# Kernel optimization log

Measured on AMD Instinct MI355X. Metric: run time of the kernel, lower is better.

The kernel has to match this reference:

```python
import jax, jax.numpy as jnp
import numpy as np

N, E, H, C, G = 10000, 20000, 12, 768, 64  # nodes, edges, heads, per-head dim, graphs
NEG_SLOPE = 0.2


def _gat_layer(x, W, a_src, a_dst, b, src, dst):
    # x: [N, 768], W: [768, H*C], a_src/a_dst: [H, C], b: [C]
    h = (x @ W).reshape(-1, H, C)                      # [N, H, C]
    s = jnp.einsum('nhc,hc->nh', h, a_src)             # alpha_src per node
    d = jnp.einsum('nhc,hc->nh', h, a_dst)             # alpha_dst per node
    e = jax.nn.leaky_relu(s[src] + d[dst], NEG_SLOPE)  # [Etot, H]
    # segment softmax over incoming edges of each destination node
    m = jax.lax.stop_gradient(jax.ops.segment_max(e, dst, num_segments=N))
    ex = jnp.exp(e - m[dst])
    den = jax.ops.segment_sum(ex, dst, num_segments=N)
    alpha = ex / (den[dst] + 1e-16)                    # [Etot, H]
    out = jax.ops.segment_sum(h[src] * alpha[:, :, None], dst, num_segments=N)
    return out.mean(axis=1) + b                        # concat=False -> head mean, [N, C]


def setup_inputs() -> dict:
    key = jax.random.key(0)
    ks = jax.random.split(key, 16)
    sc = 0.02
    f32 = jnp.float32
    return {
        'x': jax.random.normal(ks[0], (N, 768), f32),
        'edge_index': jax.random.randint(ks[1], (2, E), 0, N),
        'batch': jnp.sort(jax.random.randint(ks[2], (N,), 0, G)),
        'W1': (jax.random.normal(ks[3], (768, H * C), f32) * sc),
        'a_src1': (jax.random.normal(ks[4], (H, C), f32) * sc),
        'a_dst1': (jax.random.normal(ks[5], (H, C), f32) * sc),
        'b1': jnp.zeros((C,), f32),
        'W2': (jax.random.normal(ks[6], (768, H * C), f32) * sc),
        'a_src2': (jax.random.normal(ks[7], (H, C), f32) * sc),
        'a_dst2': (jax.random.normal(ks[8], (H, C), f32) * sc),
        'b2': jnp.zeros((C,), f32),
        'mlp_w1': (jax.random.normal(ks[9], (768, 128), f32) * sc),
        'mlp_b1': jnp.zeros((128,), f32),
        'mlp_w2': (jax.random.normal(ks[10], (128, 4), f32) * sc),
        'mlp_b2': jnp.zeros((4,), f32),
    }


def reference(x, edge_index, batch, W1, a_src1, a_dst1, b1, W2, a_src2, a_dst2, b2,
              mlp_w1, mlp_b1, mlp_w2, mlp_b2):
    loops = jnp.arange(N)                               # GATConv add_self_loops=True
    src = jnp.concatenate([edge_index[0], loops])
    dst = jnp.concatenate([edge_index[1], loops])
    h = _gat_layer(x, W1, a_src1, a_dst1, b1, src, dst)
    h = _gat_layer(h, W2, a_src2, a_dst2, b2, src, dst)
    # scatter_mean over graph assignment
    ssum = jax.ops.segment_sum(h, batch, num_segments=G)
    cnt = jax.ops.segment_sum(jnp.ones((N,), h.dtype), batch, num_segments=G)
    g = ssum / jnp.maximum(cnt, 1.0)[:, None]           # [G, 768]
    z = jax.nn.relu(g @ mlp_w1 + mlp_b1)
    return z @ mlp_w2 + mlp_b2                          # [G, 4] logits
```

## Files before the change

### kernel.cpp

```cpp
#include <hip/hip_runtime.h>
#include <stdint.h>

typedef unsigned short u16;
typedef unsigned int   u32;

#define NNODES 10000
#define NEDGES 20000
#define ETOT   30000
#define NHEADS 12
#define CDIM   768
#define FDIM   768
#define KDIM   9216
#define NGRAPH 64
#define MPAD   10240
#define SPLITS 4
#define KCH    (KDIM / SPLITS)
#define NEG_SLOPE 0.2f
#define DMAX   32

typedef __attribute__((ext_vector_type(8))) short short8;
typedef __attribute__((ext_vector_type(4))) float f32x4;

__device__ __forceinline__ u16 f32_bf16(float f) {
  u32 u = __float_as_uint(f);
  u = (u + 0x7FFFu + ((u >> 16) & 1u)) >> 16;
  return (u16)u;
}

__global__ void k_count(const int* __restrict__ dste, int* __restrict__ counts) {
  int e = blockIdx.x * blockDim.x + threadIdx.x;
  if (e >= ETOT) return;
  int dst;
  if (e < NEDGES) dst = dste[e]; else dst = e - NEDGES;
  atomicAdd(&counts[dst], 1);
}

__global__ void k_scan(const int* __restrict__ counts, int* __restrict__ offs) {
  __shared__ int part[256];
  int t = threadIdx.x;
  const int chunk = 40;
  int beg = t * chunk;
  int end = beg + chunk; if (end > NNODES) end = NNODES;
  int s = 0;
  for (int i = beg; i < end && i < NNODES; i++) s += counts[i];
  part[t] = s;
  __syncthreads();
  for (int d = 1; d < 256; d <<= 1) {
    int v = (t >= d) ? part[t - d] : 0;
    __syncthreads();
    part[t] += v;
    __syncthreads();
  }
  int base = (t == 0) ? 0 : part[t - 1];
  for (int i = beg; i < end && i < NNODES; i++) { offs[i] = base; base += counts[i]; }
  if (t == 255) offs[NNODES] = base;
}

__global__ void k_seed(const int* __restrict__ offs, int* __restrict__ cursor) {
  int n = blockIdx.x * blockDim.x + threadIdx.x;
  if (n < NNODES) cursor[n] = offs[n];
}

__global__ void k_scatter(const int* __restrict__ dste, int* __restrict__ cursor,
                          int* __restrict__ elist) {
  int e = blockIdx.x * blockDim.x + threadIdx.x;
  if (e >= ETOT) return;
  int dst;
  if (e < NEDGES) dst = dste[e]; else dst = e - NEDGES;
  int pos = atomicAdd(&cursor[dst], 1);
  elist[pos] = e;
}

__global__ void k_U(const float* __restrict__ W, const float* __restrict__ a_src,
                    const float* __restrict__ a_dst, float* __restrict__ Ut) {
  int k = blockIdx.x;
  int t = threadIdx.x, w = t >> 6, l = t & 63;
  const float* Wrow = W + (size_t)k * KDIM;
#pragma unroll
  for (int q = 0; q < 6; q++) {
    int o = w * 6 + q;
    int h = (o < 12) ? o : o - 12;
    const float* av = (o < 12) ? (a_src + h * CDIM) : (a_dst + h * CDIM);
    const float* wr = Wrow + h * CDIM;
    float p = 0.f;
    for (int c = l; c < CDIM; c += 64) p += wr[c] * av[c];
#pragma unroll
    for (int d = 32; d > 0; d >>= 1) p += __shfl_down(p, d, 64);
    if (l == 0) Ut[o * FDIM + k] = p;
  }
}

__global__ void k_sd(const float* __restrict__ xin, const float* __restrict__ Ut,
                     float* __restrict__ sd) {
  __shared__ float UtS[24 * FDIM];
  int t = threadIdx.x, w = t >> 6, l = t & 63;
  const float4* U4 = (const float4*)Ut;
  float4* S4 = (float4*)UtS;
  for (int i = t; i < 24 * FDIM / 4; i += 256) S4[i] = U4[i];
  __syncthreads();
#pragma unroll
  for (int rep = 0; rep < 5; rep++) {
    int n = blockIdx.x * 20 + w * 5 + rep;
    if (n >= NNODES) continue;
    const float* xr = xin + (size_t)n * FDIM;
    float4 x0 = *(const float4*)(xr + 4 * l);
    float4 x1 = *(const float4*)(xr + 4 * l + 256);
    float4 x2 = *(const float4*)(xr + 4 * l + 512);
#pragma unroll
    for (int o = 0; o < 24; o++) {
      const float4* up = (const float4*)(UtS + o * FDIM + 4 * l);
      float4 u0 = up[0];
      float4 u1 = up[64];
      float4 u2 = up[128];
      float a = x0.x * u0.x + x0.y * u0.y + x0.z * u0.z + x0.w * u0.w
              + x1.x * u1.x + x1.y * u1.y + x1.z * u1.z + x1.w * u1.w
              + x2.x * u2.x + x2.y * u2.y + x2.z * u2.z + x2.w * u2.w;
#pragma unroll
      for (int d = 32; d > 0; d >>= 1) a += __shfl_xor(a, d, 64);
      if (l == 0) sd[n * 24 + o] = a;
    }
  }
}

__global__ void k_trans(const float* __restrict__ W, u16* __restrict__ Bt) {
  int h = blockIdx.z;
  int kt = blockIdx.x * 32, ct = blockIdx.y * 32;
  int tx = threadIdx.x, ty = threadIdx.y;
  __shared__ float tile[32][33];
#pragma unroll
  for (int r = 0; r < 4; r++)
    tile[ty + 8 * r][tx] = W[(size_t)(kt + ty + 8 * r) * KDIM + h * CDIM + ct + tx];
  __syncthreads();
#pragma unroll
  for (int r = 0; r < 4; r++)
    Bt[(size_t)(ct + ty + 8 * r) * KDIM + h * CDIM + kt + tx] = f32_bf16(tile[tx][ty + 8 * r]);
}

__global__ void k_att(const float* __restrict__ xin, const int* __restrict__ ei,
                      const int* __restrict__ offs, const int* __restrict__ elist,
                      const float* __restrict__ sd, u16* __restrict__ agg) {
  int t = threadIdx.x, w = t >> 6, l = t & 63;
  int n = blockIdx.x * 4 + w;
  __shared__ int   srcsS[4][DMAX];
  __shared__ float alphS[4][NHEADS * DMAX];
  if (n >= NNODES) return;
  int* srcs = srcsS[w];
  float* alph = alphS[w];
  int beg = offs[n];
  int deg = offs[n + 1] - beg;
  if (deg > DMAX) deg = DMAX;
  if (l < deg) {
    int e = elist[beg + l];
    srcs[l] = (e < NEDGES) ? ei[e] : e - NEDGES;
  }
  __builtin_amdgcn_wave_barrier();
  for (int p = l; p < deg * NHEADS; p += 64) {
    int i = p / NHEADS, h = p - i * NHEADS;
    float v = sd[srcs[i] * 24 + h] + sd[n * 24 + 12 + h];
    v = (v > 0.f) ? v : NEG_SLOPE * v;
    alph[h * DMAX + i] = v;
  }
  __builtin_amdgcn_wave_barrier();
  if (l < NHEADS) {
    float m = -1e30f;
    for (int i = 0; i < deg; i++) m = fmaxf(m, alph[l * DMAX + i]);
    float s = 0.f;
    for (int i = 0; i < deg; i++) {
      float ex = expf(alph[l * DMAX + i] - m);
      alph[l * DMAX + i] = ex;
      s += ex;
    }
    float inv = 1.f / (s + 1e-16f);
    for (int i = 0; i < deg; i++) alph[l * DMAX + i] *= inv;
  }
  __builtin_amdgcn_wave_barrier();
  u16* outr = agg + (size_t)n * KDIM + 4 * l;
#pragma unroll
  for (int pass = 0; pass < 3; pass++) {
    float4 acc[NHEADS];
#pragma unroll
    for (int h = 0; h < NHEADS; h++) acc[h] = make_float4(0.f, 0.f, 0.f, 0.f);
    for (int i = 0; i < deg; i++) {
      float4 xv = *(const float4*)(xin + (size_t)srcs[i] * FDIM + pass * 256 + 4 * l);
#pragma unroll
      for (int h = 0; h < NHEADS; h++) {
        float a = alph[h * DMAX + i];
        acc[h].x += a * xv.x; acc[h].y += a * xv.y;
        acc[h].z += a * xv.z; acc[h].w += a * xv.w;
      }
    }
#pragma unroll
    for (int h = 0; h < NHEADS; h++) {
      ushort4 pk;
      pk.x = f32_bf16(acc[h].x); pk.y = f32_bf16(acc[h].y);
      pk.z = f32_bf16(acc[h].z); pk.w = f32_bf16(acc[h].w);
      *(ushort4*)(outr + h * CDIM + pass * 256) = pk;
    }
  }
}

__global__ __launch_bounds__(256, 3) void k_gemm(const u16* __restrict__ A,
    const u16* __restrict__ B, float* __restrict__ C,
    const float* __restrict__ bias, float scale) {
  __shared__ __align__(16) u16 As[2][128 * 32];
  __shared__ __align__(16) u16 Bs[2][128 * 32];
  int t = threadIdx.x;
  int w = t >> 6, l = t & 63;
  int lin = blockIdx.x;
  int xcd = lin & 7;
  int s = lin >> 3;
  int kz = xcd >> 1;
  int colt = (xcd & 1) * 3 + (s % 3);
  int y = s / 3;
  int col0 = colt * 128;
  int row0 = y * 128;
  int kbeg = kz * KCH;
  int wm = (w >> 1) * 64, wn = (w & 1) * 64;
  f32x4 acc[4][4] = {};
  int idx0 = t * 8;
  int idx1 = idx0 + 2048;
  const u16* Ag0 = A + (size_t)(row0 + (idx0 >> 5)) * KDIM + (idx0 & 31) + kbeg;
  const u16* Ag1 = A + (size_t)(row0 + (idx1 >> 5)) * KDIM + (idx1 & 31) + kbeg;
  const u16* Bg0 = B + (size_t)(col0 + (idx0 >> 5)) * KDIM + (idx0 & 31) + kbeg;
  const u16* Bg1 = B + (size_t)(col0 + (idx1 >> 5)) * KDIM + (idx1 & 31) + kbeg;
  int lr = l & 15, lk = (l >> 4) * 8;

  short8 ra0, ra1, rb0, rb1;
  auto gload = [&](int k0) {
    ra0 = *(const short8*)(Ag0 + k0);
    ra1 = *(const short8*)(Ag1 + k0);
    rb0 = *(const short8*)(Bg0 + k0);
    rb1 = *(const short8*)(Bg1 + k0);
  };
  auto swrite = [&](int buf) {
    *(short8*)(&As[buf][idx0]) = ra0;
    *(short8*)(&As[buf][idx1]) = ra1;
    *(short8*)(&Bs[buf][idx0]) = rb0;
    *(short8*)(&Bs[buf][idx1]) = rb1;
  };

  gload(0);
  swrite(0);
  gload(32);
  __syncthreads();
  const int NIT = KCH / 32;
  int cur = 0;
  for (int it = 0; it < NIT; it++) {
    short8 af[4], bf[4];
#pragma unroll
    for (int i = 0; i < 4; i++) af[i] = *(const short8*)(&As[cur][(wm + i * 16 + lr) * 32 + lk]);
#pragma unroll
    for (int j = 0; j < 4; j++) bf[j] = *(const short8*)(&Bs[cur][(wn + j * 16 + lr) * 32 + lk]);
#pragma unroll
    for (int i = 0; i < 4; i++)
#pragma unroll
      for (int j = 0; j < 4; j++)
        acc[i][j] = __builtin_amdgcn_mfma_f32_16x16x32_bf16(af[i], bf[j], acc[i][j], 0, 0, 0);
    if (it + 1 < NIT) {
      swrite(cur ^ 1);
      if (it + 2 < NIT) gload((it + 2) * 32);
    }
    __syncthreads();
    cur ^= 1;
  }

  int lg = l >> 4;
#pragma unroll
  for (int i = 0; i < 4; i++)
#pragma unroll
    for (int j = 0; j < 4; j++) {
      int col = col0 + wn + j * 16 + lr;
      float badd = (kz == 0) ? bias[col] : 0.f;
#pragma unroll
      for (int r = 0; r < 4; r++) {
        int row = row0 + wm + i * 16 + lg * 4 + r;
        unsafeAtomicAdd(&C[(size_t)row * FDIM + col], acc[i][j][r] * scale + badd);
      }
    }
}

__global__ void k_pool(const float* __restrict__ h2, const int* __restrict__ batch,
                       float* __restrict__ g) {
  int gi = blockIdx.x;
  int c = blockIdx.y * 256 + threadIdx.x;
  int lo = 0, hi = NNODES;
  while (lo < hi) { int mid = (lo + hi) >> 1; if (batch[mid] < gi) lo = mid + 1; else hi = mid; }
  int start = lo;
  lo = start; hi = NNODES;
  while (lo < hi) { int mid = (lo + hi) >> 1; if (batch[mid] < gi + 1) lo = mid + 1; else hi = mid; }
  int end = lo;
  int cnt = end - start; if (cnt < 1) cnt = 1;
  float inv = 1.f / (float)cnt;
  float s = 0.f;
  for (int n = start; n < end; n++) s += h2[(size_t)n * FDIM + c];
  g[gi * FDIM + c] = s * inv;
}

__global__ void k_mlp(const float* __restrict__ g, const float* __restrict__ w1,
                      const float* __restrict__ b1, const float* __restrict__ w2,
                      const float* __restrict__ b2, float* __restrict__ out) {
  int gi = blockIdx.x;
  int t = threadIdx.x;
  __shared__ float gs[FDIM];
  __shared__ float zs[128];
  for (int i = t; i < FDIM; i += 128) gs[i] = g[gi * FDIM + i];
  __syncthreads();
  float a = b1[t];
  for (int k = 0; k < FDIM; k++) a += gs[k] * w1[k * 128 + t];
  zs[t] = (a > 0.f) ? a : 0.f;
  __syncthreads();
  if (t < 4) {
    float o = b2[t];
    for (int i = 0; i < 128; i++) o += zs[i] * w2[i * 4 + t];
    out[gi * 4 + t] = o;
  }
}

extern "C" void kernel_launch(void* const* d_in, const int* in_sizes, int n_in,
                              void* d_out, int out_size, void* d_ws, size_t ws_size,
                              hipStream_t stream) {
  const float* x    = (const float*)d_in[0];
  const int*   ei   = (const int*)d_in[1];
  const int*   batch= (const int*)d_in[2];
  const float* W1   = (const float*)d_in[3];
  const float* as1  = (const float*)d_in[4];
  const float* ad1  = (const float*)d_in[5];
  const float* b1   = (const float*)d_in[6];
  const float* W2   = (const float*)d_in[7];
  const float* as2  = (const float*)d_in[8];
  const float* ad2  = (const float*)d_in[9];
  const float* b2   = (const float*)d_in[10];
  const float* mw1  = (const float*)d_in[11];
  const float* mb1  = (const float*)d_in[12];
  const float* mw2  = (const float*)d_in[13];
  const float* mb2  = (const float*)d_in[14];
  float* out = (float*)d_out;
  (void)in_sizes; (void)n_in; (void)out_size; (void)ws_size;

  char* wsb = (char*)d_ws;
  size_t off = 0;
  auto alloc = [&](size_t bytes) -> void* {
    void* p = wsb + off;
    off += (bytes + 255) & ~(size_t)255;
    return p;
  };
  u16*  agg    = (u16*)alloc((size_t)MPAD * KDIM * 2);
  u16*  Bt     = (u16*)alloc((size_t)FDIM * KDIM * 2);
  float* h1    = (float*)alloc((size_t)MPAD * FDIM * 4);
  float* h2    = (float*)alloc((size_t)MPAD * FDIM * 4);
  float* sd    = (float*)alloc((size_t)NNODES * 24 * 4);
  float* Ut    = (float*)alloc((size_t)FDIM * 24 * 4);
  int*  counts = (int*)alloc((size_t)NNODES * 4);
  int*  offs   = (int*)alloc((size_t)(NNODES + 1) * 4);
  int*  cursor = (int*)alloc((size_t)NNODES * 4);
  int*  elist  = (int*)alloc((size_t)ETOT * 4);
  float* gbuf  = (float*)alloc((size_t)NGRAPH * FDIM * 4);

  hipMemsetAsync(counts, 0, NNODES * 4, stream);
  k_count<<<(ETOT + 255) / 256, 256, 0, stream>>>(ei + NEDGES, counts);
  k_scan<<<1, 256, 0, stream>>>(counts, offs);
  k_seed<<<(NNODES + 255) / 256, 256, 0, stream>>>(offs, cursor);
  k_scatter<<<(ETOT + 255) / 256, 256, 0, stream>>>(ei + NEDGES, cursor, elist);

  for (int layer = 0; layer < 2; layer++) {
    const float* xin  = layer ? h1  : x;
    const float* W    = layer ? W2  : W1;
    const float* asrc = layer ? as2 : as1;
    const float* adst = layer ? ad2 : ad1;
    const float* bb   = layer ? b2  : b1;
    float* hout       = layer ? h2  : h1;

    k_U<<<FDIM, 256, 0, stream>>>(W, asrc, adst, Ut);
    k_sd<<<(NNODES + 19) / 20, 256, 0, stream>>>(xin, Ut, sd);
    k_trans<<<dim3(24, 24, 12), dim3(32, 8), 0, stream>>>(W, Bt);
    hipMemsetAsync(hout, 0, (size_t)MPAD * FDIM * 4, stream);
    k_att<<<(NNODES + 3) / 4, 256, 0, stream>>>(xin, ei, offs, elist, sd, agg);
    k_gemm<<<1920, 256, 0, stream>>>(agg, Bt, hout, bb, 1.f / 12.f);
  }

  k_pool<<<dim3(NGRAPH, 3), 256, 0, stream>>>(h2, batch, gbuf);
  k_mlp<<<NGRAPH, 128, 0, stream>>>(gbuf, mw1, mb1, mw2, mb2, out);
}
```

Baseline: 949.2 us.

## Reorder GAT layer to project features before attention aggregation

Projects node features first (x in bf16 times W, giving a bf16 [N, 9216] per-head feature matrix). Attention then gathers these projected per-head rows, does the head-mean and adds the bias directly. This removes the split-K GEMM with float atomics and the output memset. The cost is that the gather now reads full 9216-wide bf16 rows per edge instead of 768-wide fp32 rows, which raises gather traffic. It also rounds the input to bf16 before the projection.

```diff
diff --git a/kernel.cpp b/kernel.cpp
--- a/kernel.cpp
+++ b/kernel.cpp
@@ -12,9 +12,7 @@
 #define FDIM   768
 #define KDIM   9216
 #define NGRAPH 64
-#define MPAD   10240
-#define SPLITS 4
-#define KCH    (KDIM / SPLITS)
+#define MPAD   10112
 #define NEG_SLOPE 0.2f
 #define DMAX   32
 
@@ -25,6 +23,9 @@
   u32 u = __float_as_uint(f);
   u = (u + 0x7FFFu + ((u >> 16) & 1u)) >> 16;
   return (u16)u;
+}
+__device__ __forceinline__ float bf16_f32(u16 v) {
+  return __uint_as_float(((u32)v) << 16);
 }
 
 __global__ void k_count(const int* __restrict__ dste, int* __restrict__ counts) {
@@ -91,7 +92,7 @@
 }
 
 __global__ void k_sd(const float* __restrict__ xin, const float* __restrict__ Ut,
-                     float* __restrict__ sd) {
+                     float* __restrict__ sd, u16* __restrict__ xbf) {
   __shared__ float UtS[24 * FDIM];
   int t = threadIdx.x, w = t >> 6, l = t & 63;
   const float4* U4 = (const float4*)Ut;
@@ -106,6 +107,14 @@
     float4 x0 = *(const float4*)(xr + 4 * l);
     float4 x1 = *(const float4*)(xr + 4 * l + 256);
     float4 x2 = *(const float4*)(xr + 4 * l + 512);
+    u16* xb = xbf + (size_t)n * FDIM + 4 * l;
+    ushort4 p0, p1, p2;
+    p0.x = f32_bf16(x0.x); p0.y = f32_bf16(x0.y); p0.z = f32_bf16(x0.z); p0.w = f32_bf16(x0.w);
+    p1.x = f32_bf16(x1.x); p1.y = f32_bf16(x1.y); p1.z = f32_bf16(x1.z); p1.w = f32_bf16(x1.w);
+    p2.x = f32_bf16(x2.x); p2.y = f32_bf16(x2.y); p2.z = f32_bf16(x2.z); p2.w = f32_bf16(x2.w);
+    *(ushort4*)xb = p0;
+    *(ushort4*)(xb + 256) = p1;
+    *(ushort4*)(xb + 512) = p2;
 #pragma unroll
     for (int o = 0; o < 24; o++) {
       const float4* up = (const float4*)(UtS + o * FDIM + 4 * l);
@@ -123,22 +132,93 @@
 }
 
 __global__ void k_trans(const float* __restrict__ W, u16* __restrict__ Bt) {
-  int h = blockIdx.z;
-  int kt = blockIdx.x * 32, ct = blockIdx.y * 32;
+  int kt = blockIdx.x * 32, jt = blockIdx.y * 32;
   int tx = threadIdx.x, ty = threadIdx.y;
   __shared__ float tile[32][33];
 #pragma unroll
   for (int r = 0; r < 4; r++)
-    tile[ty + 8 * r][tx] = W[(size_t)(kt + ty + 8 * r) * KDIM + h * CDIM + ct + tx];
+    tile[ty + 8 * r][tx] = W[(size_t)(kt + ty + 8 * r) * KDIM + jt + tx];
   __syncthreads();
 #pragma unroll
   for (int r = 0; r < 4; r++)
-    Bt[(size_t)(ct + ty + 8 * r) * KDIM + h * CDIM + kt + tx] = f32_bf16(tile[tx][ty + 8 * r]);
-}
-
-__global__ void k_att(const float* __restrict__ xin, const int* __restrict__ ei,
+    Bt[(size_t)(jt + ty + 8 * r) * FDIM + kt + tx] = f32_bf16(tile[tx][ty + 8 * r]);
+}
+
+__global__ __launch_bounds__(256, 3) void k_gemm(const u16* __restrict__ A,
+    const u16* __restrict__ B, u16* __restrict__ C) {
+  __shared__ __align__(16) u16 As[2][128 * 32];
+  __shared__ __align__(16) u16 Bs[2][128 * 32];
+  int t = threadIdx.x;
+  int w = t >> 6, l = t & 63;
+  int col0 = blockIdx.x * 128;
+  int row0 = blockIdx.y * 128;
+  int wm = (w >> 1) * 64, wn = (w & 1) * 64;
+  f32x4 acc[4][4] = {};
+  int idx0 = t * 8;
+  int idx1 = idx0 + 2048;
+  const u16* Ag0 = A + (size_t)(row0 + (idx0 >> 5)) * FDIM + (idx0 & 31);
+  const u16* Ag1 = A + (size_t)(row0 + (idx1 >> 5)) * FDIM + (idx1 & 31);
+  const u16* Bg0 = B + (size_t)(col0 + (idx0 >> 5)) * FDIM + (idx0 & 31);
+  const u16* Bg1 = B + (size_t)(col0 + (idx1 >> 5)) * FDIM + (idx1 & 31);
+  int lr = l & 15, lk = (l >> 4) * 8;
+
+  short8 ra0, ra1, rb0, rb1;
+  auto gload = [&](int k0) {
+    ra0 = *(const short8*)(Ag0 + k0);
+    ra1 = *(const short8*)(Ag1 + k0);
+    rb0 = *(const short8*)(Bg0 + k0);
+    rb1 = *(const short8*)(Bg1 + k0);
+  };
+  auto swrite = [&](int buf) {
+    *(short8*)(&As[buf][idx0]) = ra0;
+    *(short8*)(&As[buf][idx1]) = ra1;
+    *(short8*)(&Bs[buf][idx0]) = rb0;
+    *(short8*)(&Bs[buf][idx1]) = rb1;
+  };
+
+  gload(0);
+  swrite(0);
+  gload(32);
+  __syncthreads();
+  const int NIT = FDIM / 32;
+  int cur = 0;
+  for (int it = 0; it < NIT; it++) {
+    short8 af[4], bf[4];
+#pragma unroll
+    for (int i = 0; i < 4; i++) af[i] = *(const short8*)(&As[cur][(wm + i * 16 + lr) * 32 + lk]);
+#pragma unroll
+    for (int j = 0; j < 4; j++) bf[j] = *(const short8*)(&Bs[cur][(wn + j * 16 + lr) * 32 + lk]);
+#pragma unroll
+    for (int i = 0; i < 4; i++)
+#pragma unroll
+      for (int j = 0; j < 4; j++)
+        acc[i][j] = __builtin_amdgcn_mfma_f32_16x16x32_bf16(af[i], bf[j], acc[i][j], 0, 0, 0);
+    if (it + 1 < NIT) {
+      swrite(cur ^ 1);
+      if (it + 2 < NIT) gload((it + 2) * 32);
+    }
+    __syncthreads();
+    cur ^= 1;
+  }
+
+  int lg = l >> 4;
+#pragma unroll
+  for (int i = 0; i < 4; i++)
+#pragma unroll
+    for (int j = 0; j < 4; j++) {
+      int col = col0 + wn + j * 16 + lr;
+#pragma unroll
+      for (int r = 0; r < 4; r++) {
+        int row = row0 + wm + i * 16 + lg * 4 + r;
+        C[(size_t)row * KDIM + col] = f32_bf16(acc[i][j][r]);
+      }
+    }
+}
+
+__global__ void k_att(const u16* __restrict__ Hbig, const int* __restrict__ ei,
                       const int* __restrict__ offs, const int* __restrict__ elist,
-                      const float* __restrict__ sd, u16* __restrict__ agg) {
+                      const float* __restrict__ sd, const float* __restrict__ bias,
+                      float* __restrict__ out) {
   int t = threadIdx.x, w = t >> 6, l = t & 63;
   int n = blockIdx.x * 4 + w;
   __shared__ int   srcsS[4][DMAX];
@@ -174,109 +254,30 @@
     for (int i = 0; i < deg; i++) alph[l * DMAX + i] *= inv;
   }
   __builtin_amdgcn_wave_barrier();
-  u16* outr = agg + (size_t)n * KDIM + 4 * l;
 #pragma unroll
   for (int pass = 0; pass < 3; pass++) {
-    float4 acc[NHEADS];
-#pragma unroll
-    for (int h = 0; h < NHEADS; h++) acc[h] = make_float4(0.f, 0.f, 0.f, 0.f);
+    float4 acc = make_float4(0.f, 0.f, 0.f, 0.f);
     for (int i = 0; i < deg; i++) {
-      float4 xv = *(const float4*)(xin + (size_t)srcs[i] * FDIM + pass * 256 + 4 * l);
+      const u16* hb = Hbig + (size_t)srcs[i] * KDIM + pass * 256 + 4 * l;
 #pragma unroll
       for (int h = 0; h < NHEADS; h++) {
+        ushort4 hv = *(const ushort4*)(hb + h * CDIM);
         float a = alph[h * DMAX + i];
-        acc[h].x += a * xv.x; acc[h].y += a * xv.y;
-        acc[h].z += a * xv.z; acc[h].w += a * xv.w;
+        acc.x += a * bf16_f32(hv.x);
+        acc.y += a * bf16_f32(hv.y);
+        acc.z += a * bf16_f32(hv.z);
+        acc.w += a * bf16_f32(hv.w);
       }
     }
-#pragma unroll
-    for (int h = 0; h < NHEADS; h++) {
-      ushort4 pk;
-      pk.x = f32_bf16(acc[h].x); pk.y = f32_bf16(acc[h].y);
-      pk.z = f32_bf16(acc[h].z); pk.w = f32_bf16(acc[h].w);
-      *(ushort4*)(outr + h * CDIM + pass * 256) = pk;
-    }
-  }
-}
-
-__global__ __launch_bounds__(256, 3) void k_gemm(const u16* __restrict__ A,
-    const u16* __restrict__ B, float* __restrict__ C,
-    const float* __restrict__ bias, float scale) {
-  __shared__ __align__(16) u16 As[2][128 * 32];
-  __shared__ __align__(16) u16 Bs[2][128 * 32];
-  int t = threadIdx.x;
-  int w = t >> 6, l = t & 63;
-  int lin = blockIdx.x;
-  int xcd = lin & 7;
-  int s = lin >> 3;
-  int kz = xcd >> 1;
-  int colt = (xcd & 1) * 3 + (s % 3);
-  int y = s / 3;
-  int col0 = colt * 128;
-  int row0 = y * 128;
-  int kbeg = kz * KCH;
-  int wm = (w >> 1) * 64, wn = (w & 1) * 64;
-  f32x4 acc[4][4] = {};
-  int idx0 = t * 8;
-  int idx1 = idx0 + 2048;
-  const u16* Ag0 = A + (size_t)(row0 + (idx0 >> 5)) * KDIM + (idx0 & 31) + kbeg;
-  const u16* Ag1 = A + (size_t)(row0 + (idx1 >> 5)) * KDIM + (idx1 & 31) + kbeg;
-  const u16* Bg0 = B + (size_t)(col0 + (idx0 >> 5)) * KDIM + (idx0 & 31) + kbeg;
-  const u16* Bg1 = B + (size_t)(col0 + (idx1 >> 5)) * KDIM + (idx1 & 31) + kbeg;
-  int lr = l & 15, lk = (l >> 4) * 8;
-
-  short8 ra0, ra1, rb0, rb1;
-  auto gload = [&](int k0) {
-    ra0 = *(const short8*)(Ag0 + k0);
-    ra1 = *(const short8*)(Ag1 + k0);
-    rb0 = *(const short8*)(Bg0 + k0);
-    rb1 = *(const short8*)(Bg1 + k0);
-  };
-  auto swrite = [&](int buf) {
-    *(short8*)(&As[buf][idx0]) = ra0;
-    *(short8*)(&As[buf][idx1]) = ra1;
-    *(short8*)(&Bs[buf][idx0]) = rb0;
-    *(short8*)(&Bs[buf][idx1]) = rb1;
-  };
-
-  gload(0);
-  swrite(0);
-  gload(32);
-  __syncthreads();
-  const int NIT = KCH / 32;
-  int cur = 0;
-  for (int it = 0; it < NIT; it++) {
-    short8 af[4], bf[4];
-#pragma unroll
-    for (int i = 0; i < 4; i++) af[i] = *(const short8*)(&As[cur][(wm + i * 16 + lr) * 32 + lk]);
-#pragma unroll
-    for (int j = 0; j < 4; j++) bf[j] = *(const short8*)(&Bs[cur][(wn + j * 16 + lr) * 32 + lk]);
-#pragma unroll
-    for (int i = 0; i < 4; i++)
-#pragma unroll
-      for (int j = 0; j < 4; j++)
-        acc[i][j] = __builtin_amdgcn_mfma_f32_16x16x32_bf16(af[i], bf[j], acc[i][j], 0, 0, 0);
-    if (it + 1 < NIT) {
-      swrite(cur ^ 1);
-      if (it + 2 < NIT) gload((it + 2) * 32);
-    }
-    __syncthreads();
-    cur ^= 1;
-  }
-
-  int lg = l >> 4;
-#pragma unroll
-  for (int i = 0; i < 4; i++)
-#pragma unroll
-    for (int j = 0; j < 4; j++) {
-      int col = col0 + wn + j * 16 + lr;
-      float badd = (kz == 0) ? bias[col] : 0.f;
-#pragma unroll
-      for (int r = 0; r < 4; r++) {
-        int row = row0 + wm + i * 16 + lg * 4 + r;
-        unsafeAtomicAdd(&C[(size_t)row * FDIM + col], acc[i][j][r] * scale + badd);
-      }
-    }
+    int c = pass * 256 + 4 * l;
+    const float sc = 1.f / 12.f;
+    float4 ov;
+    ov.x = acc.x * sc + bias[c + 0];
+    ov.y = acc.y * sc + bias[c + 1];
+    ov.z = acc.z * sc + bias[c + 2];
+    ov.w = acc.w * sc + bias[c + 3];
+    *(float4*)(out + (size_t)n * FDIM + c) = ov;
+  }
 }
 
 __global__ void k_pool(const float* __restrict__ h2, const int* __restrict__ batch,
@@ -344,10 +345,11 @@
     off += (bytes + 255) & ~(size_t)255;
     return p;
   };
-  u16*  agg    = (u16*)alloc((size_t)MPAD * KDIM * 2);
-  u16*  Bt     = (u16*)alloc((size_t)FDIM * KDIM * 2);
-  float* h1    = (float*)alloc((size_t)MPAD * FDIM * 4);
-  float* h2    = (float*)alloc((size_t)MPAD * FDIM * 4);
+  u16*  Hbig   = (u16*)alloc((size_t)MPAD * KDIM * 2);
+  u16*  Bt     = (u16*)alloc((size_t)KDIM * FDIM * 2);
+  float* h1    = (float*)alloc((size_t)NNODES * FDIM * 4);
+  float* h2    = (float*)alloc((size_t)NNODES * FDIM * 4);
+  u16*  xbf    = (u16*)h2;
   float* sd    = (float*)alloc((size_t)NNODES * 24 * 4);
   float* Ut    = (float*)alloc((size_t)FDIM * 24 * 4);
   int*  counts = (int*)alloc((size_t)NNODES * 4);
@@ -371,11 +373,10 @@
     float* hout       = layer ? h2  : h1;
 
     k_U<<<FDIM, 256, 0, stream>>>(W, asrc, adst, Ut);
-    k_sd<<<(NNODES + 19) / 20, 256, 0, stream>>>(xin, Ut, sd);
-    k_trans<<<dim3(24, 24, 12), dim3(32, 8), 0, stream>>>(W, Bt);
-    hipMemsetAsync(hout, 0, (size_t)MPAD * FDIM * 4, stream);
-    k_att<<<(NNODES + 3) / 4, 256, 0, stream>>>(xin, ei, offs, elist, sd, agg);
-    k_gemm<<<1920, 256, 0, stream>>>(agg, Bt, hout, bb, 1.f / 12.f);
+    k_sd<<<(NNODES + 19) / 20, 256, 0, stream>>>(xin, Ut, sd, xbf);
+    k_trans<<<dim3(FDIM / 32, KDIM / 32), dim3(32, 8), 0, stream>>>(W, Bt);
+    k_gemm<<<dim3(KDIM / 128, MPAD / 128), 256, 0, stream>>>(xbf, Bt, Hbig);
+    k_att<<<(NNODES + 3) / 4, 256, 0, stream>>>(Hbig, ei, offs, elist, sd, bb, hout);
   }
 
   k_pool<<<dim3(NGRAPH, 3), 256, 0, stream>>>(h2, batch, gbuf);
```

After: 913.7 us. -3.7%, faster.
